# Kernel tuning notes

Measured on AMD Instinct MI355X. Metric: run time of the kernel, lower is better.

## Reference

```python
import jax, jax.numpy as jnp
import numpy as np

IN_FEATURES = 1024
OUT_FEATURES = 256
NUM_KNOTS = 10
SPLINE_ORDER = 3
NUM_BASIS = NUM_KNOTS + SPLINE_ORDER  # 13
EPS = 1e-8


def setup_inputs() -> dict:
    key = jax.random.key(0)
    k1, k2 = jax.random.split(key)
    x = jax.random.normal(k1, (8192, IN_FEATURES), dtype=jnp.float32)
    spline_coeffs = jax.random.normal(
        k2, (OUT_FEATURES, IN_FEATURES, NUM_BASIS), dtype=jnp.float32) * 0.1
    knots = jnp.linspace(-1.0, 1.0, NUM_KNOTS + 2 * SPLINE_ORDER, dtype=jnp.float32)
    return {"x": x, "spline_coeffs": spline_coeffs, "knots": knots}


def _basis_functions(x, knots):
    # x: (B, I) already tanh-normalized; returns (B, I, NUM_BASIS)
    xc = jnp.clip(x, -1.0, 1.0)[..., None]          # (B, I, 1)
    left = knots[:NUM_BASIS - 1]                     # (nb-1,)
    center = knots[1:NUM_BASIS]                      # (nb-1,)
    right = knots[2:NUM_BASIS + 1]                   # (nb-1,)  (i+2 < len(knots) always)
    mask_l = (xc >= left) & (xc < center)
    mask_r = (xc >= center) & (xc < right)
    up = mask_l.astype(xc.dtype) * (xc - left) / (center - left + EPS)
    down = mask_r.astype(xc.dtype) * (right - xc) / (right - center + EPS)
    b = up + down                                    # (B, I, nb-1)
    # last basis column is never written in the original loop -> zeros
    return jnp.pad(b, ((0, 0), (0, 0), (0, 1)))


def reference(x, spline_coeffs, knots):
    x_norm = jnp.tanh(x)
    basis = _basis_functions(x_norm, knots)          # (B, I, K)
    # output[b, j] = sum_i sum_k basis[b, i, k] * coeffs[j, i, k]
    return jnp.einsum('bik,jik->bj', basis, spline_coeffs)
```

## Files before the change

### kernel.cpp

```cpp
#include <hip/hip_runtime.h>
#include <cstdint>
#include <cstddef>


typedef _Float16 half2_v __attribute__((ext_vector_type(2)));
typedef __fp16  fp16x2  __attribute__((ext_vector_type(2)));
typedef _Float16 f16x8 __attribute__((ext_vector_type(8)));
typedef float f32x4 __attribute__((ext_vector_type(4)));

__device__ __forceinline__ half2_v u32_as_h2(uint32_t u) {
  union { uint32_t u; half2_v h; } c; c.u = u; return c.h;
}
__device__ __forceinline__ uint32_t h2_as_u32(half2_v h) {
  union { uint32_t u; half2_v h; } c; c.h = h; return c.u;
}
__device__ __forceinline__ half2_v cvt_pk_h2(float a, float b) {
  union { fp16x2 f; half2_v h; } c;
  c.f = __builtin_amdgcn_cvt_pkrtz(a, b);
  return c.h;
}
__device__ __forceinline__ float dot2f(half2_v a, half2_v b, float c) {
#if __has_builtin(__builtin_amdgcn_fdot2)
  return __builtin_amdgcn_fdot2(a, b, c, false);
#else
  return c + (float)a[0] * (float)b[0] + (float)a[1] * (float)b[1];
#endif
}
__device__ __forceinline__ uint16_t f16_bits(float v) {
  union { _Float16 h; uint16_t u; } c; c.h = (_Float16)v; return c.u;
}

__device__ __forceinline__ float fast_tanhf(float v) {
  const float e = __expf(2.0f * v);
  return 1.0f - 2.0f / (e + 1.0f);
}

#define KSTEP 0.13333333333333333f
#define KINV  7.49999943750004f
__device__ __forceinline__ void kan_weights(float xin, float& w0, float& w1, int& lo) {
  float xc = fast_tanhf(xin);
  xc = fminf(fmaxf(xc, -1.0f), 1.0f);
  int m = (int)((xc + 1.0f) * 7.5f);
  m = min(max(m, 0), 14);
  const float k0 = fmaf((float)m, KSTEP, -1.0f);
  const float up = (xc - k0) * KINV;
  const float dn = (k0 + KSTEP - xc) * KINV;
  w0 = (m == 0) ? up : ((m <= 12) ? dn : 0.0f);
  w1 = (m >= 1 && m <= 11) ? up : 0.0f;
  lo = min(max(m - 1, 0), 11);
}

__device__ __forceinline__ void load_lds16(const void* g, void* l) {
  __builtin_amdgcn_global_load_lds((const __attribute__((address_space(1))) void*)g,
                                   (__attribute__((address_space(3))) void*)l, 16, 0, 0);
}

#define GMM 8192
#define GNN 256
#define KI  16
#define GK2 (1024 * KI)
#define KSPL2 8
#define IPER (1024 / KSPL2)
#define BM2 256
#define BN2 256
#define NIT (IPER / 4)

__global__ __launch_bounds__(256)
void kan_prep_B2(const float* __restrict__ coef, uint32_t* __restrict__ B2) {
  const int tid = blockIdx.x * 256 + threadIdx.x;
  const float* cp = coef + (size_t)tid * 13;
  uint32_t w[8];
#pragma unroll
  for (int q = 0; q < 6; ++q) w[q] = h2_as_u32(cvt_pk_h2(cp[2 * q], cp[2 * q + 1]));
  w[6] = 0u; w[7] = 0u;
  uint4* p = (uint4*)(B2 + (size_t)tid * 8);
  p[0] = make_uint4(w[0], w[1], w[2], w[3]);
  p[1] = make_uint4(w[4], w[5], w[6], w[7]);
}

__global__ __launch_bounds__(512, 2)
void kan_gemm7(const float* __restrict__ x, const _Float16* __restrict__ B2,
               float* __restrict__ out) {
  __shared__ __align__(16) char Bs[2][BN2 * 128];
  __shared__ __align__(16) char As[2][4 * BM2 * 32];

  const int t    = threadIdx.x;
  const int lane = t & 63;
  const int wv   = t >> 6;
  const int mw   = wv & 1;
  const int nw   = wv >> 1;
  const int fr   = lane & 15;
  const int fq   = lane >> 4;
  const int m0   = blockIdx.z * BM2;
  const int i00  = blockIdx.x * IPER;
  const int fr_swz = ((fr >> 2) & 1) * 16;
  const int a_half = (fq & 1) * 16;

  f32x4 acc[8][4];
#pragma unroll
  for (int a = 0; a < 8; ++a)
#pragma unroll
    for (int b = 0; b < 4; ++b) acc[a][b] = (f32x4){0.f, 0.f, 0.f, 0.f};

  const int sn[4] = { (0 * 512 + t) >> 3, (1 * 512 + t) >> 3,
                      (2 * 512 + t) >> 3, (3 * 512 + t) >> 3 };
  const int sc = t & 7;
  const int p_row = t & 255;
  const int p_ip  = (t >> 8) * 2;
  const int p_swz = ((p_row >> 2) & 1) * 16;
  const float* xrow = x + (size_t)(m0 + p_row) * 1024 + p_ip;

  auto stageB = [&](int it) {
    const _Float16* Bb = B2 + (size_t)(i00 + it * 4) * KI;
    char* Bd = (char*)Bs[it & 1];
#pragma unroll
    for (int s = 0; s < 4; ++s) {
      const int c = sc ^ (sn[s] & 7);
      load_lds16(Bb + (size_t)sn[s] * GK2 + c * 8, Bd + (s * 512 + t) * 16);
    }
  };
  auto loadx = [&](int it) -> float2 {
    return *(const float2*)(xrow + i00 + it * 4);
  };
  auto expand = [&](int it, float2 xv) {
    char* Ab = As[it & 1];
#pragma unroll
    for (int d = 0; d < 2; ++d) {
      float w0, w1; int lo;
      kan_weights(d ? xv.y : xv.x, w0, w1, lo);
      const uint32_t wp  = (uint32_t)f16_bits(w0) | ((uint32_t)f16_bits(w1) << 16);
      const uint32_t wlo = (lo & 1) ? (wp << 16) : wp;
      const uint32_t whi = (lo & 1) ? (wp >> 16) : 0u;
      const int w = lo >> 1;
      char* rb = Ab + (size_t)((p_ip + d) * BM2 + p_row) * 32;
      *(uint4*)(rb + p_swz)        = make_uint4(0u, 0u, 0u, 0u);
      *(uint4*)(rb + (p_swz ^ 16)) = make_uint4(0u, 0u, 0u, 0u);
      *(uint32_t*)(rb + (((w + 1) * 4) ^ p_swz)) = whi;
      *(uint32_t*)(rb + ((w * 4) ^ p_swz))       = wlo;
    }
  };

  float2 xc = loadx(0);
  stageB(0);
  expand(0, xc);
  float2 xn = loadx(1);

  for (int it = 0; it < NIT; ++it) {
    __syncthreads();

    if (it + 1 < NIT) {
      stageB(it + 1);
      expand(it + 1, xn);
      if (it + 2 < NIT) xn = loadx(it + 2);
    }

    const char* Bd = (const char*)Bs[it & 1];
    const char* Ad = (const char*)As[it & 1];
#pragma unroll
    for (int ks = 0; ks < 2; ++ks) {
      const int iloc = ks * 2 + (fq >> 1);
      f16x8 bf[4];
#pragma unroll
      for (int ni = 0; ni < 4; ++ni) {
        const int row = nw * 64 + ni * 16 + fr;
        bf[ni] = *(const f16x8*)(Bd + (row * 8 + ((ks * 4 + fq) ^ (row & 7))) * 16);
      }
#pragma unroll
      for (int mi = 0; mi < 8; ++mi) {
        const f16x8 af = *(const f16x8*)(Ad +
            (size_t)((iloc * BM2 + mw * 128 + mi * 16 + fr) * 32) + (a_half ^ fr_swz));
#pragma unroll
        for (int ni = 0; ni < 4; ++ni)
          acc[mi][ni] = __builtin_amdgcn_mfma_f32_16x16x32_f16(af, bf[ni], acc[mi][ni], 0, 0, 0);
      }
    }
  }

#pragma unroll
  for (int mi = 0; mi < 8; ++mi) {
    const int gr = m0 + mw * 128 + mi * 16 + fq * 4;
#pragma unroll
    for (int ni = 0; ni < 4; ++ni) {
      const int gc = nw * 64 + ni * 16 + fr;
#pragma unroll
      for (int r = 0; r < 4; ++r)
        atomicAdd(&out[(size_t)(gr + r) * GNN + gc], acc[mi][ni][r]);
    }
  }
}

#define TI 8
#define BT 256
#define JT 32
#define ISPL 2
#define IRANGE (1024 / ISPL)

__global__ __launch_bounds__(256)
void kan_dot2(const float* __restrict__ x, const float* __restrict__ coef,
              float* __restrict__ out) {
  __shared__ uint32_t Plds[TI * 12 * JT];
  const int t    = threadIdx.x;
  const int b    = blockIdx.x * BT + t;
  const int j0   = blockIdx.y * JT;
  const int cbeg = blockIdx.z * (IRANGE / TI);

  float acc[JT];
#pragma unroll
  for (int q = 0; q < JT; ++q) acc[q] = 0.0f;

  const int s_jj   = t & 31;
  const int s_iloc = t >> 5;

  for (int c = cbeg; c < cbeg + IRANGE / TI; ++c) {
    const int i0 = c * TI;
    __syncthreads();
    {
      const float* cp0 = coef + ((size_t)(j0 + s_jj) * 1024 + (i0 + s_iloc)) * 13;
      float cv[13];
#pragma unroll
      for (int s = 0; s < 13; ++s) cv[s] = cp0[s];
#pragma unroll
      for (int r = 0; r < 12; ++r) {
        half2_v h; h[0] = (_Float16)cv[r]; h[1] = (_Float16)cv[r + 1];
        const int slot = ((s_jj >> 2) + r) & 7;
        Plds[(s_iloc * 12 + r) * 32 + slot * 4 + (s_jj & 3)] = h2_as_u32(h);
      }
    }
    uint32_t wr[TI]; int lor[TI];
    {
      const float* xr = x + (size_t)b * 1024 + i0;
      const float4 xa = *(const float4*)(xr);
      const float4 xb = *(const float4*)(xr + 4);
      const float xv[TI] = {xa.x, xa.y, xa.z, xa.w, xb.x, xb.y, xb.z, xb.w};
#pragma unroll
      for (int q = 0; q < TI; ++q) {
        float w0, w1; int lo;
        kan_weights(xv[q], w0, w1, lo);
        wr[q] = (uint32_t)f16_bits(w0) | ((uint32_t)f16_bits(w1) << 16);
        lor[q] = lo;
      }
    }
    __syncthreads();

    const uint4* P4 = (const uint4*)Plds;
#pragma unroll
    for (int ii = 0; ii < TI; ++ii) {
      const half2_v hw = u32_as_h2(wr[ii]);
      const int lo = lor[ii];
      const int base = (ii * 12 + lo) * 8;
#pragma unroll
      for (int g = 0; g < 8; ++g) {
        const uint4 v = P4[base + ((g + lo) & 7)];
        acc[4 * g + 0] = dot2f(hw, u32_as_h2(v.x), acc[4 * g + 0]);
        acc[4 * g + 1] = dot2f(hw, u32_as_h2(v.y), acc[4 * g + 1]);
        acc[4 * g + 2] = dot2f(hw, u32_as_h2(v.z), acc[4 * g + 2]);
        acc[4 * g + 3] = dot2f(hw, u32_as_h2(v.w), acc[4 * g + 3]);
      }
    }
  }

  float* orow = out + (size_t)b * 256 + j0;
#pragma unroll
  for (int q = 0; q < JT; ++q) atomicAdd(orow + q, acc[q]);
}

extern "C" void kernel_launch(void* const* d_in, const int* in_sizes, int n_in,
                              void* d_out, int out_size, void* d_ws, size_t ws_size,
                              hipStream_t stream) {
  const float* x     = (const float*)d_in[0];
  const float* coef  = (const float*)d_in[1];
  float* out = (float*)d_out;

  (void)hipMemsetAsync(out, 0, (size_t)out_size * sizeof(float), stream);

  const size_t nB2 = (size_t)GNN * GK2;
  if (ws_size >= nB2 * 2) {
    _Float16* B2 = (_Float16*)d_ws;
    kan_prep_B2<<<(int)((size_t)GNN * 1024 / 256), 256, 0, stream>>>(coef, (uint32_t*)B2);
    dim3 grid(KSPL2, 1, GMM / BM2);
    kan_gemm7<<<grid, 512, 0, stream>>>(x, B2, out);
  } else {
    dim3 grid(8192 / BT, 256 / JT, ISPL);
    kan_dot2<<<grid, 256, 0, stream>>>(x, coef, out);
  }
}
```

Measured before the change: 194.0 us.

## Interleave LDS reads, global staging and MFMA clusters; fuse output zeroing into prep

Each K iteration of the GEMM is split into four phases. Each phase reads one half of the A or B fragments from LDS, issues part of the next tile's global-to-LDS loads or A expansion, then runs a 16-MFMA cluster at raised priority, with barriers between phases. The aim is to hide staging and expansion latency under matrix-core work instead of doing all staging up front. It also removes the separate memset by zeroing the output inside the coefficient prep kernel, which saves one launch but relies on prep's thread count matching the output size.

Result: slower. 198.9 us (+2.5%).

```diff
diff --git a/kernel.cpp b/kernel.cpp
--- a/kernel.cpp
+++ b/kernel.cpp
@@ -66,7 +66,8 @@
 #define NIT (IPER / 4)
 
 __global__ __launch_bounds__(256)
-void kan_prep_B2(const float* __restrict__ coef, uint32_t* __restrict__ B2) {
+void kan_prep_B2(const float* __restrict__ coef, uint32_t* __restrict__ B2,
+                 float4* __restrict__ outz) {
   const int tid = blockIdx.x * 256 + threadIdx.x;
   const float* cp = coef + (size_t)tid * 13;
   uint32_t w[8];
@@ -76,10 +77,13 @@
   uint4* p = (uint4*)(B2 + (size_t)tid * 8);
   p[0] = make_uint4(w[0], w[1], w[2], w[3]);
   p[1] = make_uint4(w[4], w[5], w[6], w[7]);
+  const float4 z = make_float4(0.f, 0.f, 0.f, 0.f);
+  outz[tid] = z;
+  outz[tid + 262144] = z;
 }
 
 __global__ __launch_bounds__(512, 2)
-void kan_gemm7(const float* __restrict__ x, const _Float16* __restrict__ B2,
+void kan_gemm9(const float* __restrict__ x, const _Float16* __restrict__ B2,
                float* __restrict__ out) {
   __shared__ __align__(16) char Bs[2][BN2 * 128];
   __shared__ __align__(16) char As[2][4 * BM2 * 32];
@@ -110,71 +114,102 @@
   const int p_swz = ((p_row >> 2) & 1) * 16;
   const float* xrow = x + (size_t)(m0 + p_row) * 1024 + p_ip;
 
-  auto stageB = [&](int it) {
-    const _Float16* Bb = B2 + (size_t)(i00 + it * 4) * KI;
-    char* Bd = (char*)Bs[it & 1];
-#pragma unroll
-    for (int s = 0; s < 4; ++s) {
-      const int c = sc ^ (sn[s] & 7);
-      load_lds16(Bb + (size_t)sn[s] * GK2 + c * 8, Bd + (s * 512 + t) * 16);
-    }
+  auto stage1 = [&](const _Float16* Bb, char* Bnx, int s) {
+    const int c = sc ^ (sn[s] & 7);
+    load_lds16(Bb + (size_t)sn[s] * GK2 + c * 8, Bnx + (s * 512 + t) * 16);
   };
   auto loadx = [&](int it) -> float2 {
     return *(const float2*)(xrow + i00 + it * 4);
   };
-  auto expand = [&](int it, float2 xv) {
-    char* Ab = As[it & 1];
-#pragma unroll
-    for (int d = 0; d < 2; ++d) {
-      float w0, w1; int lo;
-      kan_weights(d ? xv.y : xv.x, w0, w1, lo);
-      const uint32_t wp  = (uint32_t)f16_bits(w0) | ((uint32_t)f16_bits(w1) << 16);
-      const uint32_t wlo = (lo & 1) ? (wp << 16) : wp;
-      const uint32_t whi = (lo & 1) ? (wp >> 16) : 0u;
-      const int w = lo >> 1;
-      char* rb = Ab + (size_t)((p_ip + d) * BM2 + p_row) * 32;
-      *(uint4*)(rb + p_swz)        = make_uint4(0u, 0u, 0u, 0u);
-      *(uint4*)(rb + (p_swz ^ 16)) = make_uint4(0u, 0u, 0u, 0u);
-      *(uint32_t*)(rb + (((w + 1) * 4) ^ p_swz)) = whi;
-      *(uint32_t*)(rb + ((w * 4) ^ p_swz))       = wlo;
-    }
+  auto expand_half = [&](char* Anx, float xv, int d) {
+    float w0, w1; int lo;
+    kan_weights(xv, w0, w1, lo);
+    const uint32_t wp  = (uint32_t)f16_bits(w0) | ((uint32_t)f16_bits(w1) << 16);
+    const uint32_t wlo = (lo & 1) ? (wp << 16) : wp;
+    const uint32_t whi = (lo & 1) ? (wp >> 16) : 0u;
+    const int w = lo >> 1;
+    char* rb = Anx + (size_t)((p_ip + d) * BM2 + p_row) * 32;
+    *(uint4*)(rb + p_swz)        = make_uint4(0u, 0u, 0u, 0u);
+    *(uint4*)(rb + (p_swz ^ 16)) = make_uint4(0u, 0u, 0u, 0u);
+    *(uint32_t*)(rb + (((w + 1) * 4) ^ p_swz)) = whi;
+    *(uint32_t*)(rb + ((w * 4) ^ p_swz))       = wlo;
   };
 
+#define MFMA_CLUSTER(MH)                                                        \
+  __builtin_amdgcn_s_barrier();                                                 \
+  asm volatile("s_waitcnt lgkmcnt(0)" ::: "memory");                            \
+  __builtin_amdgcn_sched_barrier(0);                                            \
+  __builtin_amdgcn_s_setprio(1);                                                \
+  _Pragma("unroll")                                                             \
+  for (int q = 0; q < 4; ++q)                                                   \
+    _Pragma("unroll")                                                           \
+    for (int ni = 0; ni < 4; ++ni)                                              \
+      acc[(MH) * 4 + q][ni] = __builtin_amdgcn_mfma_f32_16x16x32_f16(           \
+          af[q], bf[ni], acc[(MH) * 4 + q][ni], 0, 0, 0);                       \
+  __builtin_amdgcn_s_setprio(0);
+
   float2 xc = loadx(0);
-  stageB(0);
-  expand(0, xc);
-  float2 xn = loadx(1);
+  {
+    const _Float16* Bb0 = B2 + (size_t)i00 * KI;
+    char* B0 = (char*)Bs[0];
+#pragma unroll
+    for (int s = 0; s < 4; ++s) stage1(Bb0, B0, s);
+  }
+  expand_half((char*)As[0], xc.x, 0);
+  expand_half((char*)As[0], xc.y, 1);
+  xc = loadx(1);
+  __syncthreads();
 
   for (int it = 0; it < NIT; ++it) {
-    __syncthreads();
-
-    if (it + 1 < NIT) {
-      stageB(it + 1);
-      expand(it + 1, xn);
-      if (it + 2 < NIT) xn = loadx(it + 2);
-    }
-
-    const char* Bd = (const char*)Bs[it & 1];
-    const char* Ad = (const char*)As[it & 1];
-#pragma unroll
-    for (int ks = 0; ks < 2; ++ks) {
-      const int iloc = ks * 2 + (fq >> 1);
-      f16x8 bf[4];
+    const int cur = it & 1;
+    const char* Bd = (const char*)Bs[cur];
+    const char* Ad = (const char*)As[cur];
+    char* Bnx = (char*)Bs[cur ^ 1];
+    char* Anx = (char*)As[cur ^ 1];
+    const bool pre = (it + 1 < NIT);
+    const _Float16* Bb = B2 + (size_t)(i00 + (it + 1) * 4) * KI;
+
+    f16x8 af[4], bf[4];
+    float2 xn;
+
+    auto rd_b = [&](int ks) {
 #pragma unroll
       for (int ni = 0; ni < 4; ++ni) {
         const int row = nw * 64 + ni * 16 + fr;
         bf[ni] = *(const f16x8*)(Bd + (row * 8 + ((ks * 4 + fq) ^ (row & 7))) * 16);
       }
-#pragma unroll
-      for (int mi = 0; mi < 8; ++mi) {
-        const f16x8 af = *(const f16x8*)(Ad +
-            (size_t)((iloc * BM2 + mw * 128 + mi * 16 + fr) * 32) + (a_half ^ fr_swz));
-#pragma unroll
-        for (int ni = 0; ni < 4; ++ni)
-          acc[mi][ni] = __builtin_amdgcn_mfma_f32_16x16x32_f16(af, bf[ni], acc[mi][ni], 0, 0, 0);
-      }
-    }
-  }
+    };
+    auto rd_a = [&](int ks, int mh) {
+      const int iloc = ks * 2 + (fq >> 1);
+#pragma unroll
+      for (int q = 0; q < 4; ++q)
+        af[q] = *(const f16x8*)(Ad +
+            (size_t)((iloc * BM2 + mw * 128 + mh * 64 + q * 16 + fr) * 32) +
+            (a_half ^ fr_swz));
+    };
+
+    rd_b(0); rd_a(0, 0);
+    if (pre) { stage1(Bb, Bnx, 0); stage1(Bb, Bnx, 1); }
+    xn = loadx((it + 2 < NIT) ? it + 2 : NIT - 1);
+    MFMA_CLUSTER(0)
+    __builtin_amdgcn_s_barrier();
+
+    rd_a(0, 1);
+    if (pre) { stage1(Bb, Bnx, 2); expand_half(Anx, xc.x, 0); }
+    MFMA_CLUSTER(1)
+    __builtin_amdgcn_s_barrier();
+
+    rd_b(1); rd_a(1, 0);
+    if (pre) { stage1(Bb, Bnx, 3); expand_half(Anx, xc.y, 1); }
+    MFMA_CLUSTER(0)
+    __builtin_amdgcn_s_barrier();
+
+    rd_a(1, 1);
+    MFMA_CLUSTER(1)
+    xc = xn;
+    __syncthreads();
+  }
+#undef MFMA_CLUSTER
 
 #pragma unroll
   for (int mi = 0; mi < 8; ++mi) {
@@ -271,15 +306,15 @@
   const float* coef  = (const float*)d_in[1];
   float* out = (float*)d_out;
 
-  (void)hipMemsetAsync(out, 0, (size_t)out_size * sizeof(float), stream);
-
   const size_t nB2 = (size_t)GNN * GK2;
   if (ws_size >= nB2 * 2) {
     _Float16* B2 = (_Float16*)d_ws;
-    kan_prep_B2<<<(int)((size_t)GNN * 1024 / 256), 256, 0, stream>>>(coef, (uint32_t*)B2);
+    kan_prep_B2<<<(int)((size_t)GNN * 1024 / 256), 256, 0, stream>>>(
+        coef, (uint32_t*)B2, (float4*)out);
     dim3 grid(KSPL2, 1, GMM / BM2);
-    kan_gemm7<<<grid, 512, 0, stream>>>(x, B2, out);
+    kan_gemm9<<<grid, 512, 0, stream>>>(x, B2, out);
   } else {
+    (void)hipMemsetAsync(out, 0, (size_t)out_size * sizeof(float), stream);
     dim3 grid(8192 / BT, 256 / JT, ISPL);
     kan_dot2<<<grid, 256, 0, stream>>>(x, coef, out);
   }
```

## Rewrite spline GEMM with smaller M tile, deeper B pipeline, fused output zeroing

Applied to the files above, without the earlier changes.

Replaces the GEMM kernel with one that uses a 128-row M tile, a 4-stage ring buffer of B tiles in LDS and a finer per-input granule schedule. Explicit waitcnt and barriers let loads and expansion overlap MFMA work, and setprio raises wave priority around the MFMA block. The output zeroing moves from hipMemsetAsync into the prep kernel, which removes one launch. The smaller tile doubles the number of blocks, so more atomic adds go to the output, but occupancy (launch bounds 4) goes up.

Result: no change. 193.2 us (-0.4%).

```diff
diff --git a/kernel.cpp b/kernel.cpp
--- a/kernel.cpp
+++ b/kernel.cpp
@@ -61,12 +61,14 @@
 #define GK2 (1024 * KI)
 #define KSPL2 8
 #define IPER (1024 / KSPL2)
-#define BM2 256
+#define BM2 128
 #define BN2 256
-#define NIT (IPER / 4)
+#define NGRAN 64
+#define NBODY 16
 
 __global__ __launch_bounds__(256)
-void kan_prep_B2(const float* __restrict__ coef, uint32_t* __restrict__ B2) {
+void kan_prep_B2(const float* __restrict__ coef, uint32_t* __restrict__ B2,
+                 float4* __restrict__ outz) {
   const int tid = blockIdx.x * 256 + threadIdx.x;
   const float* cp = coef + (size_t)tid * 13;
   uint32_t w[8];
@@ -76,115 +78,138 @@
   uint4* p = (uint4*)(B2 + (size_t)tid * 8);
   p[0] = make_uint4(w[0], w[1], w[2], w[3]);
   p[1] = make_uint4(w[4], w[5], w[6], w[7]);
-}
-
-__global__ __launch_bounds__(512, 2)
-void kan_gemm7(const float* __restrict__ x, const _Float16* __restrict__ B2,
-               float* __restrict__ out) {
-  __shared__ __align__(16) char Bs[2][BN2 * 128];
-  __shared__ __align__(16) char As[2][4 * BM2 * 32];
+  const float4 z = make_float4(0.f, 0.f, 0.f, 0.f);
+  outz[tid] = z;
+  outz[tid + 262144] = z;
+}
+
+__global__ __launch_bounds__(512, 4)
+void kan_gemm10(const float* __restrict__ x, const _Float16* __restrict__ B2,
+                float* __restrict__ out) {
+  __shared__ __align__(16) char Bs[4][16384];
+  __shared__ __align__(16) char As[2][8192];
+  char* BsP = (char*)Bs;
+  char* AsP = (char*)As;
 
   const int t    = threadIdx.x;
   const int lane = t & 63;
   const int wv   = t >> 6;
-  const int mw   = wv & 1;
-  const int nw   = wv >> 1;
+  const int wm   = (wv & 1) * 64;
+  const int wn   = (wv >> 1) * 64;
   const int fr   = lane & 15;
   const int fq   = lane >> 4;
   const int m0   = blockIdx.z * BM2;
   const int i00  = blockIdx.x * IPER;
-  const int fr_swz = ((fr >> 2) & 1) * 16;
-  const int a_half = (fq & 1) * 16;
-
-  f32x4 acc[8][4];
-#pragma unroll
-  for (int a = 0; a < 8; ++a)
+
+  const int fr_swz = (((wm >> 2) + (fr >> 2)) & 1) * 16;
+  const int a_base = (wm + fr) * 32 + (((fq & 1) * 16) ^ fr_swz) + (fq >> 1) * 4096;
+  const int b_base = (wn + fr) * 64 + ((fq ^ (fr & 3)) * 16);
+
+  f32x4 acc[4][4];
+#pragma unroll
+  for (int a = 0; a < 4; ++a)
 #pragma unroll
     for (int b = 0; b < 4; ++b) acc[a][b] = (f32x4){0.f, 0.f, 0.f, 0.f};
 
-  const int sn[4] = { (0 * 512 + t) >> 3, (1 * 512 + t) >> 3,
-                      (2 * 512 + t) >> 3, (3 * 512 + t) >> 3 };
-  const int sc = t & 7;
-  const int p_row = t & 255;
-  const int p_ip  = (t >> 8) * 2;
-  const int p_swz = ((p_row >> 2) & 1) * 16;
-  const float* xrow = x + (size_t)(m0 + p_row) * 1024 + p_ip;
-
-  auto stageB = [&](int it) {
-    const _Float16* Bb = B2 + (size_t)(i00 + it * 4) * KI;
-    char* Bd = (char*)Bs[it & 1];
-#pragma unroll
-    for (int s = 0; s < 4; ++s) {
-      const int c = sc ^ (sn[s] & 7);
-      load_lds16(Bb + (size_t)sn[s] * GK2 + c * 8, Bd + (s * 512 + t) * 16);
-    }
+  const int srow0 = t >> 2, sc0 = t & 3;
+  const int srow1 = 128 + (t >> 2);
+  const _Float16* sp0 = B2 + (size_t)srow0 * GK2 + (size_t)i00 * KI
+                        + ((sc0 ^ (srow0 & 3)) * 8);
+  const _Float16* sp1 = B2 + (size_t)srow1 * GK2 + (size_t)i00 * KI
+                        + ((sc0 ^ (srow1 & 3)) * 8);
+  const int xrow   = (t >> 1) & 127;
+  const int parity = t & 1;
+  const int i_off  = (t >> 8) & 1;
+  const float* xptr = x + (size_t)(m0 + xrow) * 1024 + i00 + 2 * parity + i_off;
+  const int exp_off = (i_off * 128 + xrow) * 32;
+  const int p_swz   = ((xrow >> 2) & 1) * 16;
+
+  auto expand1 = [&](int aw, float xv) {
+    float w0, w1; int lo;
+    kan_weights(xv, w0, w1, lo);
+    const uint32_t wp  = (uint32_t)f16_bits(w0) | ((uint32_t)f16_bits(w1) << 16);
+    const uint32_t wlo = (lo & 1) ? (wp << 16) : wp;
+    const uint32_t whi = (lo & 1) ? (wp >> 16) : 0u;
+    const int w = lo >> 1;
+    char* rb = AsP + aw + exp_off;
+    *(uint4*)(rb + p_swz)        = make_uint4(0u, 0u, 0u, 0u);
+    *(uint4*)(rb + (p_swz ^ 16)) = make_uint4(0u, 0u, 0u, 0u);
+    *(uint32_t*)(rb + (((w + 1) * 4) ^ p_swz)) = whi;
+    *(uint32_t*)(rb + ((w * 4) ^ p_swz))       = wlo;
   };
-  auto loadx = [&](int it) -> float2 {
-    return *(const float2*)(xrow + i00 + it * 4);
-  };
-  auto expand = [&](int it, float2 xv) {
-    char* Ab = As[it & 1];
-#pragma unroll
-    for (int d = 0; d < 2; ++d) {
-      float w0, w1; int lo;
-      kan_weights(d ? xv.y : xv.x, w0, w1, lo);
-      const uint32_t wp  = (uint32_t)f16_bits(w0) | ((uint32_t)f16_bits(w1) << 16);
-      const uint32_t wlo = (lo & 1) ? (wp << 16) : wp;
-      const uint32_t whi = (lo & 1) ? (wp >> 16) : 0u;
-      const int w = lo >> 1;
-      char* rb = Ab + (size_t)((p_ip + d) * BM2 + p_row) * 32;
-      *(uint4*)(rb + p_swz)        = make_uint4(0u, 0u, 0u, 0u);
-      *(uint4*)(rb + (p_swz ^ 16)) = make_uint4(0u, 0u, 0u, 0u);
-      *(uint32_t*)(rb + (((w + 1) * 4) ^ p_swz)) = whi;
-      *(uint32_t*)(rb + ((w * 4) ^ p_swz))       = wlo;
-    }
-  };
-
-  float2 xc = loadx(0);
-  stageB(0);
-  expand(0, xc);
-  float2 xn = loadx(1);
-
-  for (int it = 0; it < NIT; ++it) {
-    __syncthreads();
-
-    if (it + 1 < NIT) {
-      stageB(it + 1);
-      expand(it + 1, xn);
-      if (it + 2 < NIT) xn = loadx(it + 2);
-    }
-
-    const char* Bd = (const char*)Bs[it & 1];
-    const char* Ad = (const char*)As[it & 1];
-#pragma unroll
-    for (int ks = 0; ks < 2; ++ks) {
-      const int iloc = ks * 2 + (fq >> 1);
-      f16x8 bf[4];
-#pragma unroll
-      for (int ni = 0; ni < 4; ++ni) {
-        const int row = nw * 64 + ni * 16 + fr;
-        bf[ni] = *(const f16x8*)(Bd + (row * 8 + ((ks * 4 + fq) ^ (row & 7))) * 16);
-      }
-#pragma unroll
-      for (int mi = 0; mi < 8; ++mi) {
-        const f16x8 af = *(const f16x8*)(Ad +
-            (size_t)((iloc * BM2 + mw * 128 + mi * 16 + fr) * 32) + (a_half ^ fr_swz));
-#pragma unroll
-        for (int ni = 0; ni < 4; ++ni)
-          acc[mi][ni] = __builtin_amdgcn_mfma_f32_16x16x32_f16(af, bf[ni], acc[mi][ni], 0, 0, 0);
-      }
-    }
-  }
-
-#pragma unroll
-  for (int mi = 0; mi < 8; ++mi) {
-    const int gr = m0 + mw * 128 + mi * 16 + fq * 4;
+
+  float xa, xb, xn1, xn2;
+
+  xa = xptr[0];
+  xb = xptr[4];
+  load_lds16(sp0, BsP + 0 + t * 16);
+  load_lds16(sp1, BsP + 0 + 8192 + t * 16);
+  sp0 += 32; sp1 += 32;
+  load_lds16(sp0, BsP + 16384 + t * 16);
+  load_lds16(sp1, BsP + 16384 + 8192 + t * 16);
+  sp0 += 32; sp1 += 32;
+  if (parity == 0) expand1(0, xa);
+  asm volatile("s_waitcnt vmcnt(2) lgkmcnt(0)" ::: "memory");
+  __builtin_amdgcn_s_barrier();
+  __builtin_amdgcn_sched_barrier(0);
+
+#define MFMA16(RS)                                                            \
+  __builtin_amdgcn_s_setprio(1);                                              \
+  _Pragma("unroll")                                                           \
+  for (int ni = 0; ni < 4; ++ni) {                                            \
+    const f16x8 bf = *(const f16x8*)(BsP + (RS) + b_base + ni * 1024);        \
+    acc[0][ni] = __builtin_amdgcn_mfma_f32_16x16x32_f16(af0, bf, acc[0][ni], 0, 0, 0); \
+    acc[1][ni] = __builtin_amdgcn_mfma_f32_16x16x32_f16(af1, bf, acc[1][ni], 0, 0, 0); \
+    acc[2][ni] = __builtin_amdgcn_mfma_f32_16x16x32_f16(af2, bf, acc[2][ni], 0, 0, 0); \
+    acc[3][ni] = __builtin_amdgcn_mfma_f32_16x16x32_f16(af3, bf, acc[3][ni], 0, 0, 0); \
+  }                                                                           \
+  __builtin_amdgcn_s_setprio(0);
+
+#define GRAN(P, XV, ADV, XLOAD)                                               \
+  {                                                                           \
+    f16x8 af0 = *(const f16x8*)(AsP + ((P) & 1) * 8192 + a_base);             \
+    f16x8 af1 = *(const f16x8*)(AsP + ((P) & 1) * 8192 + a_base + 512);       \
+    f16x8 af2 = *(const f16x8*)(AsP + ((P) & 1) * 8192 + a_base + 1024);      \
+    f16x8 af3 = *(const f16x8*)(AsP + ((P) & 1) * 8192 + a_base + 1536);      \
+    load_lds16(sp0, BsP + (((P) + 2) & 3) * 16384 + t * 16);                  \
+    load_lds16(sp1, BsP + (((P) + 2) & 3) * 16384 + 8192 + t * 16);           \
+    sp0 += (ADV); sp1 += (ADV);                                               \
+    XLOAD                                                                     \
+    if (parity == (((P) + 1) & 1)) expand1((((P) + 1) & 1) * 8192, XV);       \
+    asm volatile("s_waitcnt vmcnt(3) lgkmcnt(0)" ::: "memory");               \
+    __builtin_amdgcn_s_barrier();                                             \
+    __builtin_amdgcn_sched_barrier(0);                                        \
+    MFMA16((P) * 16384)                                                       \
+  }
+
+  for (int itw = 0; itw < NBODY; ++itw) {
+    const int g0 = 4 * itw;
+    const int adv0 = (g0 + 3 <= NGRAN - 1) ? 32 : 0;
+    const int adv1 = (g0 + 4 <= NGRAN - 1) ? 32 : 0;
+    const int adv2 = (g0 + 5 <= NGRAN - 1) ? 32 : 0;
+    const int adv3 = (g0 + 6 <= NGRAN - 1) ? 32 : 0;
+    int xw1 = 2 * itw + 2; if (xw1 > 31) xw1 = 31;
+    int xw2 = 2 * itw + 3; if (xw2 > 31) xw2 = 31;
+
+    GRAN(0, xa, adv0, { xn1 = xptr[4 * xw1]; })
+    GRAN(1, xb, adv1, { })
+    GRAN(2, xb, adv2, { xn2 = xptr[4 * xw2]; })
+    GRAN(3, xn1, adv3, { })
+
+    xa = xn1; xb = xn2;
+  }
+#undef GRAN
+#undef MFMA16
+
+#pragma unroll
+  for (int q = 0; q < 4; ++q) {
+    const int gr = m0 + wm + q * 16 + fq * 4;
 #pragma unroll
     for (int ni = 0; ni < 4; ++ni) {
-      const int gc = nw * 64 + ni * 16 + fr;
+      const int gc = wn + ni * 16 + fr;
 #pragma unroll
       for (int r = 0; r < 4; ++r)
-        atomicAdd(&out[(size_t)(gr + r) * GNN + gc], acc[mi][ni][r]);
+        atomicAdd(&out[(size_t)(gr + r) * GNN + gc], acc[q][ni][r]);
     }
   }
 }
@@ -271,15 +296,15 @@
   const float* coef  = (const float*)d_in[1];
   float* out = (float*)d_out;
 
-  (void)hipMemsetAsync(out, 0, (size_t)out_size * sizeof(float), stream);
-
   const size_t nB2 = (size_t)GNN * GK2;
   if (ws_size >= nB2 * 2) {
     _Float16* B2 = (_Float16*)d_ws;
-    kan_prep_B2<<<(int)((size_t)GNN * 1024 / 256), 256, 0, stream>>>(coef, (uint32_t*)B2);
+    kan_prep_B2<<<(int)((size_t)GNN * 1024 / 256), 256, 0, stream>>>(
+        coef, (uint32_t*)B2, (float4*)out);
     dim3 grid(KSPL2, 1, GMM / BM2);
-    kan_gemm7<<<grid, 512, 0, stream>>>(x, B2, out);
+    kan_gemm10<<<grid, 512, 0, stream>>>(x, B2, out);
   } else {
+    (void)hipMemsetAsync(out, 0, (size_t)out_size * sizeof(float), stream);
     dim3 grid(8192 / BT, 256 / JT, ISPL);
     kan_dot2<<<grid, 256, 0, stream>>>(x, coef, out);
   }
```
